# Performance work log

Hardware: AMD Instinct MI355X
Metric: run time of the kernel (lower is better)

Reference implementation:

```python
import jax, jax.numpy as jnp
import numpy as np
import math

B, N = 2, 384
TF, POS, TIME = 22, 32, 32
TPROJ = TIME + 1  # embed_fixed appends frame_mask channel
CS, CZ = 256, 128
POS_MAX, TIME_MAX = 2056.0, 10000.0
LN_EPS = 1e-5


def _index_emb(idx):
    # sinusoidal positional embedding of integer indices -> [..., POS]
    K = jnp.arange(POS // 2, dtype=jnp.float32)
    ang = idx[..., None].astype(jnp.float32) * jnp.pi / (POS_MAX ** (2.0 * K / POS))
    return jnp.concatenate([jnp.sin(ang), jnp.cos(ang)], axis=-1)


def _time_emb(t):
    # standard score-sde timestep embedding -> [M, TIME]
    half = TIME // 2
    freqs = jnp.exp(-(math.log(TIME_MAX) / (half - 1)) * jnp.arange(half, dtype=jnp.float32))
    ang = t[:, None] * freqs[None, :]
    return jnp.concatenate([jnp.sin(ang), jnp.cos(ang)], axis=-1)


def _ln(x, g, b):
    m = jnp.mean(x, axis=-1, keepdims=True)
    v = jnp.var(x, axis=-1, keepdims=True)
    return (x - m) * jax.lax.rsqrt(v + LN_EPS) * g + b


def _lin(x, W, b):
    return x @ W.T + b


def _forward(seq_idx, seq_feat, timestep, frame_mask,
             W_npos, b_npos, W_ntf, b_ntf, W_ntime, b_ntime,
             W_n1, b_n1, W_n2, b_n2, g_n, be_n,
             W_epos, b_epos, W_etf, b_etf, W_etime, b_etime,
             W_e1, b_e1, W_e2, b_e2, g_e, be_e):
    Bn, Nn = seq_idx.shape
    rel = seq_idx[:, :, None] - seq_idx[:, None, :]  # [B,N,N]
    seq_emb = _lin(_index_emb(seq_idx), W_npos, b_npos)          # [B,N,CS]
    edge_emb = _lin(_index_emb(rel), W_epos, b_epos)             # [B,N,N,CZ]
    seq_emb = seq_emb + _lin(seq_feat, W_ntf, b_ntf)
    # _cross_concat(x) @ W^T == (x @ Wl^T)[:, :, None] + (x @ Wr^T)[:, None, :] + b
    # (same math, avoids the O(N^2 * 2*TF) concatenated intermediate)
    edge_emb = edge_emb + (seq_feat @ W_etf[:, :TF].T)[:, :, None, :] \
                        + (seq_feat @ W_etf[:, TF:].T)[:, None, :, :] + b_etf
    t_res = (timestep[:, None] * frame_mask).reshape(-1)
    temb = _time_emb(t_res).reshape(Bn, Nn, TIME)
    temb = jnp.concatenate([temb, frame_mask[..., None]], axis=-1)  # embed_fixed -> TPROJ
    seq_emb = seq_emb + _lin(temb, W_ntime, b_ntime)
    edge_emb = edge_emb + (temb @ W_etime[:, :TPROJ].T)[:, :, None, :] \
                        + (temb @ W_etime[:, TPROJ:].T)[:, None, :, :] + b_etime
    # node_embedder: ReLU -> Linear -> ReLU -> Linear -> LayerNorm
    h = _lin(jax.nn.relu(seq_emb), W_n1, b_n1)
    seq_emb = _ln(_lin(jax.nn.relu(h), W_n2, b_n2), g_n, be_n)
    h = _lin(jax.nn.relu(edge_emb), W_e1, b_e1)
    edge_emb = _ln(_lin(jax.nn.relu(h), W_e2, b_e2), g_e, be_e)
    return seq_emb, edge_emb


def setup_inputs() -> dict:
    key = jax.random.key(0)
    ks = jax.random.split(key, 20)
    inp = {
        'seq_idx': jnp.sort(jax.random.randint(ks[0], (B, N), 0, 1000), axis=-1),
        'seq_feat': jax.random.normal(ks[1], (B, N, TF), dtype=jnp.float32),
        'timestep': jax.random.uniform(ks[2], (B,), dtype=jnp.float32),
        'frame_mask': jnp.ones((B, N), dtype=jnp.float32),
    }
    def lin(k, o, i):
        return 0.02 * jax.random.normal(k, (o, i), dtype=jnp.float32), jnp.zeros((o,), jnp.float32)
    inp['W_npos'], inp['b_npos'] = lin(ks[3], CS, POS)
    inp['W_ntf'], inp['b_ntf'] = lin(ks[4], CS, TF)
    inp['W_ntime'], inp['b_ntime'] = lin(ks[5], CS, TPROJ)
    inp['W_n1'], inp['b_n1'] = lin(ks[6], CS, CS)
    inp['W_n2'], inp['b_n2'] = lin(ks[7], CS, CS)
    inp['g_n'], inp['be_n'] = jnp.ones((CS,), jnp.float32), jnp.zeros((CS,), jnp.float32)
    inp['W_epos'], inp['b_epos'] = lin(ks[8], CZ, POS)
    inp['W_etf'], inp['b_etf'] = lin(ks[9], CZ, 2 * TF)
    inp['W_etime'], inp['b_etime'] = lin(ks[10], CZ, 2 * TPROJ)
    inp['W_e1'], inp['b_e1'] = lin(ks[11], CZ, CZ)
    inp['W_e2'], inp['b_e2'] = lin(ks[12], CZ, CZ)
    inp['g_e'], inp['be_e'] = jnp.ones((CZ,), jnp.float32), jnp.zeros((CZ,), jnp.float32)
    return inp


def reference(seq_idx, seq_feat, timestep, frame_mask,
              W_npos, b_npos, W_ntf, b_ntf, W_ntime, b_ntime,
              W_n1, b_n1, W_n2, b_n2, g_n, be_n,
              W_epos, b_epos, W_etf, b_etf, W_etime, b_etime,
              W_e1, b_e1, W_e2, b_e2, g_e, be_e):
    return _forward(seq_idx, seq_feat, timestep, frame_mask,
                    W_npos, b_npos, W_ntf, b_ntf, W_ntime, b_ntime,
                    W_n1, b_n1, W_n2, b_n2, g_n, be_n,
                    W_epos, b_epos, W_etf, b_etf, W_etime, b_etime,
                    W_e1, b_e1, W_e2, b_e2, g_e, be_e)
```

## Files before the change

kernel.cpp:

```cpp
#include <hip/hip_runtime.h>
#include <hip/hip_bf16.h>

#define BB 2
#define NN 384
#define TFD 22
#define POSD 32
#define TPROJ 33
#define CS 256
#define CZ 128
#define PI_F 3.14159265358979323846f

typedef __hip_bfloat16 bf16;
typedef __attribute__((ext_vector_type(8))) short short8;
typedef __attribute__((ext_vector_type(4))) float floatx4;

__device__ __forceinline__ float bfbits2f(unsigned short u) {
  unsigned v = ((unsigned)u) << 16;
  float f;
  __builtin_memcpy(&f, &v, 4);
  return f;
}
__device__ __forceinline__ unsigned short f2bf(float x) {
  bf16 h = __float2bfloat16(x);
  unsigned short u;
  __builtin_memcpy(&u, &h, 2);
  return u;
}
__device__ __forceinline__ bool probe_f32(const void* fm) {
  return *(const unsigned*)fm == 0x3F800000u;
}

#define TAB_OFF 0
#define SEQ0_OFF 262144
#define EL_OFF 458752
#define ER_OFF 557056
#define P_OFF 655360
#define WB_OFF 716288
#define pSEQF 0
#define pTS 16896
#define pFM 16898
#define pWNPOS 17666
#define pBNPOS 25858
#define pWNTF 26114
#define pBNTF 31746
#define pWNTIME 32002
#define pBNTIME 40450
#define pBN1 40706
#define pBN2 40962
#define pGN 41218
#define pBEN 41474
#define pWEPOS 41730
#define pBEPOS 45826
#define pWETF 45954
#define pBETF 51586
#define pWETIME 51714
#define pBETIME 60162
#define pBE1 60290
#define pBE2 60418
#define pGE 60546
#define pBEE 60674
#define UB_WE1 0
#define UB_WE2 16384
#define UB_WN1 32768
#define UB_WN2 98304

struct InPtrs { const void* p[28]; };

__global__ void cvt_all(InPtrs ip, float* __restrict__ ws) {
  const int idx = blockIdx.x * 256 + threadIdx.x;
  if (idx >= 224642) return;
  const int srci[27] = {1,2,3,4,5,6,7,8,9,11,13,14,15,16,17,18,19,20,21,23,25,26,27,22,24,10,12};
  const int pre[28] = {0,16896,16898,17666,25858,26114,31746,32002,40450,40706,40962,41218,41474,
                       41730,45826,45954,51586,51714,60162,60290,60418,60546,60674,60802,
                       77186,93570,159106,224642};
  const bool f32 = probe_f32(ip.p[3]);
  int e = 0;
  while (idx >= pre[e + 1]) ++e;
  const int j = idx - pre[e];
  const void* sp = ip.p[srci[e]];
  if (e < 23) {
    float v = f32 ? ((const float*)sp)[j] : bfbits2f(((const unsigned short*)sp)[j]);
    ws[P_OFF + pre[e] + j] = v;
  } else {
    const int ub[4] = {UB_WE1, UB_WE2, UB_WN1, UB_WN2};
    unsigned short* wb = (unsigned short*)(ws + WB_OFF);
    wb[ub[e - 23] + j] = f32 ? f2bf(((const float*)sp)[j]) : ((const unsigned short*)sp)[j];
  }
}

__global__ void tab_kernel(float* __restrict__ ws) {
  const float* P = ws + P_OFF;
  __shared__ float pe[POSD];
  int r = blockIdx.x, t = threadIdx.x;
  if (t < 16) {
    float ang = (float)(r - 1024) * PI_F * powf(2056.0f, -(float)t * (1.0f / 16.0f));
    pe[t] = sinf(ang);
    pe[t + 16] = cosf(ang);
  }
  __syncthreads();
  float acc = P[pBEPOS + t] + P[pBETF + t] + P[pBETIME + t];
  const float* w = P + pWEPOS + t * POSD;
#pragma unroll
  for (int k = 0; k < POSD; ++k) acc += pe[k] * w[k];
  ws[TAB_OFF + r * CZ + t] = acc;
}

__global__ void nodeprep(const int* __restrict__ seq_idx, float* __restrict__ ws) {
  const float* P = ws + P_OFF;
  __shared__ float pe[POSD];
  __shared__ float temb[TPROJ];
  __shared__ float sf[TFD];
  int bn = blockIdx.x, t = threadIdx.x;
  int b = bn / NN;
  float fm = P[pFM + bn];
  if (t < 16) {
    float idxv = (float)seq_idx[bn];
    float ang = idxv * PI_F * powf(2056.0f, -(float)t * (1.0f / 16.0f));
    pe[t] = sinf(ang);
    pe[t + 16] = cosf(ang);
    float tres = P[pTS + b] * fm;
    float freq = expf(-(logf(10000.0f) * (1.0f / 15.0f)) * (float)t);
    temb[t] = sinf(tres * freq);
    temb[t + 16] = cosf(tres * freq);
  }
  if (t == 16) temb[32] = fm;
  if (t < TFD) sf[t] = P[pSEQF + bn * TFD + t];
  __syncthreads();
  {
    int c = t;
    float acc = P[pBNPOS + c] + P[pBNTF + c] + P[pBNTIME + c];
    const float* w = P + pWNPOS + c * POSD;
#pragma unroll
    for (int k = 0; k < POSD; ++k) acc += pe[k] * w[k];
    const float* w2 = P + pWNTF + c * TFD;
#pragma unroll
    for (int k = 0; k < TFD; ++k) acc += sf[k] * w2[k];
    const float* w3 = P + pWNTIME + c * TPROJ;
#pragma unroll
    for (int k = 0; k < TPROJ; ++k) acc += temb[k] * w3[k];
    ws[SEQ0_OFF + bn * CS + c] = acc;
  }
  if (t < CZ) {
    int c = t;
    float acc = 0.0f;
    const float* w = P + pWETF + c * (2 * TFD);
#pragma unroll
    for (int k = 0; k < TFD; ++k) acc += sf[k] * w[k];
    const float* w2 = P + pWETIME + c * (2 * TPROJ);
#pragma unroll
    for (int k = 0; k < TPROJ; ++k) acc += temb[k] * w2[k];
    ws[EL_OFF + bn * CZ + c] = acc;
  } else {
    int c = t - CZ;
    float acc = 0.0f;
    const float* w = P + pWETF + c * (2 * TFD) + TFD;
#pragma unroll
    for (int k = 0; k < TFD; ++k) acc += sf[k] * w[k];
    const float* w2 = P + pWETIME + c * (2 * TPROJ) + TPROJ;
#pragma unroll
    for (int k = 0; k < TPROJ; ++k) acc += temb[k] * w2[k];
    ws[ER_OFF + bn * CZ + c] = acc;
  }
}

__global__ __launch_bounds__(256) void node_mfma(const float* __restrict__ ws,
                                                 const void* __restrict__ fmraw,
                                                 void* __restrict__ outv) {
  __shared__ __align__(16) unsigned short sA0[32][CS + 8];
  __shared__ __align__(16) unsigned short sA1[32][CS + 8];
  __shared__ float sO[32][CS + 4];
  __shared__ float sRed[32][8], sRedQ[32][8], sMu[32], sRs[32];
  const float* P = ws + P_OFF;
  const unsigned short* WB = (const unsigned short*)(ws + WB_OFF);
  const unsigned short* W1 = WB + UB_WN1;
  const unsigned short* W2 = WB + UB_WN2;
  const int row0 = blockIdx.x * 32;
  const int t = threadIdx.x;
  const int wave = t >> 6, lane = t & 63, quad = lane >> 4, l16 = lane & 15;
  {
    const float* seq0 = ws + SEQ0_OFF;
#pragma unroll
    for (int r = 0; r < 32; ++r) sA0[r][t] = f2bf(fmaxf(seq0[(row0 + r) * CS + t], 0.0f));
  }
  __syncthreads();
  short8 af[2][8];
  floatx4 acc[2][4];
#pragma unroll
  for (int mt = 0; mt < 2; ++mt)
#pragma unroll
    for (int ks = 0; ks < 8; ++ks)
      af[mt][ks] = *(const short8*)&sA0[mt * 16 + l16][ks * 32 + quad * 8];
#pragma unroll
  for (int mt = 0; mt < 2; ++mt)
#pragma unroll
    for (int n = 0; n < 4; ++n) acc[mt][n] = (floatx4){0.f, 0.f, 0.f, 0.f};
#pragma unroll
  for (int ntl = 0; ntl < 4; ++ntl) {
    int n0 = (wave * 4 + ntl) * 16;
#pragma unroll
    for (int ks = 0; ks < 8; ++ks) {
      short8 bfr = *(const short8*)&W1[(n0 + l16) * CS + ks * 32 + quad * 8];
      acc[0][ntl] = __builtin_amdgcn_mfma_f32_16x16x32_bf16(af[0][ks], bfr, acc[0][ntl], 0, 0, 0);
      acc[1][ntl] = __builtin_amdgcn_mfma_f32_16x16x32_bf16(af[1][ks], bfr, acc[1][ntl], 0, 0, 0);
    }
  }
#pragma unroll
  for (int ntl = 0; ntl < 4; ++ntl) {
    int n0 = (wave * 4 + ntl) * 16;
    float b1v = P[pBN1 + n0 + l16];
#pragma unroll
    for (int mt = 0; mt < 2; ++mt)
#pragma unroll
      for (int i = 0; i < 4; ++i)
        sA1[mt * 16 + quad * 4 + i][n0 + l16] = f2bf(fmaxf(acc[mt][ntl][i] + b1v, 0.0f));
  }
  __syncthreads();
#pragma unroll
  for (int mt = 0; mt < 2; ++mt)
#pragma unroll
    for (int ks = 0; ks < 8; ++ks)
      af[mt][ks] = *(const short8*)&sA1[mt * 16 + l16][ks * 32 + quad * 8];
#pragma unroll
  for (int mt = 0; mt < 2; ++mt)
#pragma unroll
    for (int n = 0; n < 4; ++n) acc[mt][n] = (floatx4){0.f, 0.f, 0.f, 0.f};
#pragma unroll
  for (int ntl = 0; ntl < 4; ++ntl) {
    int n0 = (wave * 4 + ntl) * 16;
#pragma unroll
    for (int ks = 0; ks < 8; ++ks) {
      short8 bfr = *(const short8*)&W2[(n0 + l16) * CS + ks * 32 + quad * 8];
      acc[0][ntl] = __builtin_amdgcn_mfma_f32_16x16x32_bf16(af[0][ks], bfr, acc[0][ntl], 0, 0, 0);
      acc[1][ntl] = __builtin_amdgcn_mfma_f32_16x16x32_bf16(af[1][ks], bfr, acc[1][ntl], 0, 0, 0);
    }
  }
#pragma unroll
  for (int ntl = 0; ntl < 4; ++ntl) {
    int n0 = (wave * 4 + ntl) * 16;
    float b2v = P[pBN2 + n0 + l16];
#pragma unroll
    for (int mt = 0; mt < 2; ++mt)
#pragma unroll
      for (int i = 0; i < 4; ++i)
        sO[mt * 16 + quad * 4 + i][n0 + l16] = acc[mt][ntl][i] + b2v;
  }
  __syncthreads();
  {
    int r = t >> 3, seg = t & 7;
    float s = 0.f, q = 0.f;
#pragma unroll
    for (int k = 0; k < 32; ++k) { float v = sO[r][seg * 32 + k]; s += v; q += v * v; }
    sRed[r][seg] = s; sRedQ[r][seg] = q;
  }
  __syncthreads();
  if (t < 32) {
    float s = 0.f, q = 0.f;
#pragma unroll
    for (int k = 0; k < 8; ++k) { s += sRed[t][k]; q += sRedQ[t][k]; }
    float mu = s * (1.0f / CS);
    float var = q * (1.0f / CS) - mu * mu;
    sMu[t] = mu; sRs[t] = rsqrtf(var + 1e-5f);
  }
  __syncthreads();
  {
    float g = P[pGN + t], be = P[pBEN + t];
    if (probe_f32(fmraw)) {
      float* o = (float*)outv;
#pragma unroll
      for (int r = 0; r < 32; ++r)
        o[(size_t)(row0 + r) * CS + t] = (sO[r][t] - sMu[r]) * sRs[r] * g + be;
    } else {
      bf16* o = (bf16*)outv;
#pragma unroll
      for (int r = 0; r < 32; ++r)
        o[(size_t)(row0 + r) * CS + t] = __float2bfloat16((sO[r][t] - sMu[r]) * sRs[r] * g + be);
    }
  }
}

__global__ __launch_bounds__(256) void edge_mfma(const int* __restrict__ seq_idx,
                                                 const float* __restrict__ ws,
                                                 const void* __restrict__ fmraw,
                                                 void* __restrict__ outv) {
  __shared__ __align__(16) unsigned short sA0[32][CZ + 8];
  __shared__ __align__(16) unsigned short sA1[32][CZ + 8];
  __shared__ float sO[32][CZ + 4];
  __shared__ int sRel[32];
  __shared__ float sRed[32][8], sRedQ[32][8], sMu[32], sRs[32];
  const float* tab = ws + TAB_OFF;
  const float* eL = ws + EL_OFF;
  const float* eR = ws + ER_OFF;
  const float* P = ws + P_OFF;
  const unsigned short* WB = (const unsigned short*)(ws + WB_OFF);
  const unsigned short* W1 = WB + UB_WE1;
  const unsigned short* W2 = WB + UB_WE2;
  const int bid = blockIdx.x;
  const int jt = bid % (NN / 32);
  const int rem = bid / (NN / 32);
  const int irow = rem % NN;
  const int b = rem / NN;
  const int j0 = jt * 32;
  const int t = threadIdx.x;
  const int wave = t >> 6, lane = t & 63, quad = lane >> 4, l16 = lane & 15;
  if (t < 32) {
    int rel = seq_idx[b * NN + irow] - seq_idx[b * NN + j0 + t] + 1024;
    sRel[t] = min(max(rel, 0), 2047);
  }
  __syncthreads();
  {
    int c = t & 127, rh = (t >> 7) * 16;
    float eLi = eL[(b * NN + irow) * CZ + c];
#pragma unroll
    for (int rr = 0; rr < 16; ++rr) {
      int r = rh + rr;
      float v = tab[sRel[r] * CZ + c] + eLi + eR[(b * NN + j0 + r) * CZ + c];
      sA0[r][c] = f2bf(fmaxf(v, 0.0f));
    }
  }
  __syncthreads();
  short8 af[2][4];
  floatx4 acc[2][2];
#pragma unroll
  for (int mt = 0; mt < 2; ++mt)
#pragma unroll
    for (int ks = 0; ks < 4; ++ks)
      af[mt][ks] = *(const short8*)&sA0[mt * 16 + l16][ks * 32 + quad * 8];
#pragma unroll
  for (int mt = 0; mt < 2; ++mt)
#pragma unroll
    for (int n = 0; n < 2; ++n) acc[mt][n] = (floatx4){0.f, 0.f, 0.f, 0.f};
#pragma unroll
  for (int ntl = 0; ntl < 2; ++ntl) {
    int n0 = (wave * 2 + ntl) * 16;
#pragma unroll
    for (int ks = 0; ks < 4; ++ks) {
      short8 bfr = *(const short8*)&W1[(n0 + l16) * CZ + ks * 32 + quad * 8];
      acc[0][ntl] = __builtin_amdgcn_mfma_f32_16x16x32_bf16(af[0][ks], bfr, acc[0][ntl], 0, 0, 0);
      acc[1][ntl] = __builtin_amdgcn_mfma_f32_16x16x32_bf16(af[1][ks], bfr, acc[1][ntl], 0, 0, 0);
    }
  }
#pragma unroll
  for (int ntl = 0; ntl < 2; ++ntl) {
    int n0 = (wave * 2 + ntl) * 16;
    float b1v = P[pBE1 + n0 + l16];
#pragma unroll
    for (int mt = 0; mt < 2; ++mt)
#pragma unroll
      for (int i = 0; i < 4; ++i)
        sA1[mt * 16 + quad * 4 + i][n0 + l16] = f2bf(fmaxf(acc[mt][ntl][i] + b1v, 0.0f));
  }
  __syncthreads();
#pragma unroll
  for (int mt = 0; mt < 2; ++mt)
#pragma unroll
    for (int ks = 0; ks < 4; ++ks)
      af[mt][ks] = *(const short8*)&sA1[mt * 16 + l16][ks * 32 + quad * 8];
#pragma unroll
  for (int mt = 0; mt < 2; ++mt)
#pragma unroll
    for (int n = 0; n < 2; ++n) acc[mt][n] = (floatx4){0.f, 0.f, 0.f, 0.f};
#pragma unroll
  for (int ntl = 0; ntl < 2; ++ntl) {
    int n0 = (wave * 2 + ntl) * 16;
#pragma unroll
    for (int ks = 0; ks < 4; ++ks) {
      short8 bfr = *(const short8*)&W2[(n0 + l16) * CZ + ks * 32 + quad * 8];
      acc[0][ntl] = __builtin_amdgcn_mfma_f32_16x16x32_bf16(af[0][ks], bfr, acc[0][ntl], 0, 0, 0);
      acc[1][ntl] = __builtin_amdgcn_mfma_f32_16x16x32_bf16(af[1][ks], bfr, acc[1][ntl], 0, 0, 0);
    }
  }
#pragma unroll
  for (int ntl = 0; ntl < 2; ++ntl) {
    int n0 = (wave * 2 + ntl) * 16;
    float b2v = P[pBE2 + n0 + l16];
#pragma unroll
    for (int mt = 0; mt < 2; ++mt)
#pragma unroll
      for (int i = 0; i < 4; ++i)
        sO[mt * 16 + quad * 4 + i][n0 + l16] = acc[mt][ntl][i] + b2v;
  }
  __syncthreads();
  {
    int r = t >> 3, seg = t & 7;
    float s = 0.f, q = 0.f;
#pragma unroll
    for (int k = 0; k < 16; ++k) { float v = sO[r][seg * 16 + k]; s += v; q += v * v; }
    sRed[r][seg] = s; sRedQ[r][seg] = q;
  }
  __syncthreads();
  if (t < 32) {
    float s = 0.f, q = 0.f;
#pragma unroll
    for (int k = 0; k < 8; ++k) { s += sRed[t][k]; q += sRedQ[t][k]; }
    float mu = s * (1.0f / CZ);
    float var = q * (1.0f / CZ) - mu * mu;
    sMu[t] = mu; sRs[t] = rsqrtf(var + 1e-5f);
  }
  __syncthreads();
  {
    int c = t & 127, rh = (t >> 7) * 16;
    float g = P[pGE + c], be = P[pBEE + c];
    size_t base = ((size_t)(b * NN + irow) * NN + j0) * CZ + c;
    if (probe_f32(fmraw)) {
      float* o = (float*)outv + (size_t)BB * NN * CS;
#pragma unroll
      for (int rr = 0; rr < 16; ++rr) {
        int r = rh + rr;
        o[base + (size_t)r * CZ] = (sO[r][c] - sMu[r]) * sRs[r] * g + be;
      }
    } else {
      bf16* o = (bf16*)outv + (size_t)BB * NN * CS;
#pragma unroll
      for (int rr = 0; rr < 16; ++rr) {
        int r = rh + rr;
        o[base + (size_t)r * CZ] = __float2bfloat16((sO[r][c] - sMu[r]) * sRs[r] * g + be);
      }
    }
  }
}

extern "C" void kernel_launch(void* const* d_in, const int* in_sizes, int n_in,
                              void* d_out, int out_size, void* d_ws, size_t ws_size,
                              hipStream_t stream) {
  (void)in_sizes; (void)n_in; (void)out_size; (void)ws_size;
  const int* seq_idx = (const int*)d_in[0];
  float* ws = (float*)d_ws;
  InPtrs ip;
  for (int i = 0; i < 28; ++i) ip.p[i] = d_in[i];
  hipLaunchKernelGGL(cvt_all, dim3(878), dim3(256), 0, stream, ip, ws);
  hipLaunchKernelGGL(tab_kernel, dim3(2048), dim3(CZ), 0, stream, ws);
  hipLaunchKernelGGL(nodeprep, dim3(BB * NN), dim3(CS), 0, stream, seq_idx, ws);
  hipLaunchKernelGGL(node_mfma, dim3(BB * NN / 32), dim3(256), 0, stream, ws, d_in[3], d_out);
  hipLaunchKernelGGL(edge_mfma, dim3(BB * NN * (NN / 32)), dim3(256), 0, stream,
                     seq_idx, ws, d_in[3], d_out);
}
```

Before: 308.4 us.

## Merge prep kernels into one launch and restructure edge MLP per-wave in registers

Folds the conversion, relative-position table and node-prep kernels into a single launch. Tab and nodeprep now read raw inputs directly instead of waiting on the converted workspace copy. The edge kernel is restructured so each wave owns 16 pair rows: it builds the MFMA operands straight from global float4 loads, keeps the hidden layer in a small per-wave LDS tile, and does the LayerNorm with wave shuffles and vectorised stores. This removes block-wide syncs and shared staging, at the cost of more registers per thread and re-reading the weights from global memory in every wave.

```diff
diff --git a/kernel.cpp b/kernel.cpp
--- a/kernel.cpp
+++ b/kernel.cpp
@@ -28,6 +28,9 @@
 }
 __device__ __forceinline__ bool probe_f32(const void* fm) {
   return *(const unsigned*)fm == 0x3F800000u;
+}
+__device__ __forceinline__ float ldraw(const void* p, int i, bool f32) {
+  return f32 ? ((const float*)p)[i] : bfbits2f(((const unsigned short*)p)[i]);
 }
 
 #define TAB_OFF 0
@@ -64,102 +67,103 @@
 #define UB_WN1 32768
 #define UB_WN2 98304
 
+#define NB_CVT 878
+#define NB_TAB 1024
+#define NB_NODEPREP 768
+
 struct InPtrs { const void* p[28]; };
 
-__global__ void cvt_all(InPtrs ip, float* __restrict__ ws) {
-  const int idx = blockIdx.x * 256 + threadIdx.x;
-  if (idx >= 224642) return;
-  const int srci[27] = {1,2,3,4,5,6,7,8,9,11,13,14,15,16,17,18,19,20,21,23,25,26,27,22,24,10,12};
-  const int pre[28] = {0,16896,16898,17666,25858,26114,31746,32002,40450,40706,40962,41218,41474,
-                       41730,45826,45954,51586,51714,60162,60290,60418,60546,60674,60802,
-                       77186,93570,159106,224642};
+__device__ const int g_srci[27] = {1,2,3,4,5,6,7,8,9,11,13,14,15,16,17,18,19,20,21,23,25,26,27,22,24,10,12};
+__device__ const int g_pre[28] = {0,16896,16898,17666,25858,26114,31746,32002,40450,40706,40962,41218,41474,
+                                  41730,45826,45954,51586,51714,60162,60290,60418,60546,60674,60802,
+                                  77186,93570,159106,224642};
+__device__ const int g_ub[4] = {UB_WE1, UB_WE2, UB_WN1, UB_WN2};
+
+__global__ __launch_bounds__(256) void prep(InPtrs ip, const int* __restrict__ seq_idx,
+                                            float* __restrict__ ws) {
   const bool f32 = probe_f32(ip.p[3]);
-  int e = 0;
-  while (idx >= pre[e + 1]) ++e;
-  const int j = idx - pre[e];
-  const void* sp = ip.p[srci[e]];
-  if (e < 23) {
-    float v = f32 ? ((const float*)sp)[j] : bfbits2f(((const unsigned short*)sp)[j]);
-    ws[P_OFF + pre[e] + j] = v;
-  } else {
-    const int ub[4] = {UB_WE1, UB_WE2, UB_WN1, UB_WN2};
-    unsigned short* wb = (unsigned short*)(ws + WB_OFF);
-    wb[ub[e - 23] + j] = f32 ? f2bf(((const float*)sp)[j]) : ((const unsigned short*)sp)[j];
-  }
-}
-
-__global__ void tab_kernel(float* __restrict__ ws) {
-  const float* P = ws + P_OFF;
-  __shared__ float pe[POSD];
-  int r = blockIdx.x, t = threadIdx.x;
-  if (t < 16) {
-    float ang = (float)(r - 1024) * PI_F * powf(2056.0f, -(float)t * (1.0f / 16.0f));
-    pe[t] = sinf(ang);
-    pe[t + 16] = cosf(ang);
-  }
-  __syncthreads();
-  float acc = P[pBEPOS + t] + P[pBETF + t] + P[pBETIME + t];
-  const float* w = P + pWEPOS + t * POSD;
-#pragma unroll
-  for (int k = 0; k < POSD; ++k) acc += pe[k] * w[k];
-  ws[TAB_OFF + r * CZ + t] = acc;
-}
-
-__global__ void nodeprep(const int* __restrict__ seq_idx, float* __restrict__ ws) {
-  const float* P = ws + P_OFF;
-  __shared__ float pe[POSD];
-  __shared__ float temb[TPROJ];
-  __shared__ float sf[TFD];
-  int bn = blockIdx.x, t = threadIdx.x;
-  int b = bn / NN;
-  float fm = P[pFM + bn];
-  if (t < 16) {
-    float idxv = (float)seq_idx[bn];
-    float ang = idxv * PI_F * powf(2056.0f, -(float)t * (1.0f / 16.0f));
-    pe[t] = sinf(ang);
-    pe[t + 16] = cosf(ang);
-    float tres = P[pTS + b] * fm;
-    float freq = expf(-(logf(10000.0f) * (1.0f / 15.0f)) * (float)t);
-    temb[t] = sinf(tres * freq);
-    temb[t + 16] = cosf(tres * freq);
-  }
-  if (t == 16) temb[32] = fm;
-  if (t < TFD) sf[t] = P[pSEQF + bn * TFD + t];
-  __syncthreads();
+  const int t = threadIdx.x;
+  int sb = blockIdx.x;
+  if (sb < NB_CVT) {
+    int idx = sb * 256 + t;
+    if (idx >= 224642) return;
+    int e = 0;
+    while (idx >= g_pre[e + 1]) ++e;
+    int j = idx - g_pre[e];
+    const void* sp = ip.p[g_srci[e]];
+    if (e < 23) {
+      ws[P_OFF + g_pre[e] + j] = ldraw(sp, j, f32);
+    } else {
+      unsigned short* wb = (unsigned short*)(ws + WB_OFF);
+      wb[g_ub[e - 23] + j] = f32 ? f2bf(((const float*)sp)[j]) : ((const unsigned short*)sp)[j];
+    }
+    return;
+  }
+  sb -= NB_CVT;
+  if (sb < NB_TAB) {
+    __shared__ float pe[2][POSD];
+    int half = t >> 7, tc = t & 127;
+    int r = sb * 2 + half;
+    if (tc < 16) {
+      float ang = (float)(r - 1024) * PI_F * powf(2056.0f, -(float)tc * (1.0f / 16.0f));
+      pe[half][tc] = sinf(ang);
+      pe[half][tc + 16] = cosf(ang);
+    }
+    __syncthreads();
+    float acc = ldraw(ip.p[17], tc, f32) + ldraw(ip.p[19], tc, f32) + ldraw(ip.p[21], tc, f32);
+#pragma unroll
+    for (int k = 0; k < POSD; ++k) acc += pe[half][k] * ldraw(ip.p[16], tc * POSD + k, f32);
+    ws[TAB_OFF + r * CZ + tc] = acc;
+    return;
+  }
+  sb -= NB_TAB;
   {
-    int c = t;
-    float acc = P[pBNPOS + c] + P[pBNTF + c] + P[pBNTIME + c];
-    const float* w = P + pWNPOS + c * POSD;
-#pragma unroll
-    for (int k = 0; k < POSD; ++k) acc += pe[k] * w[k];
-    const float* w2 = P + pWNTF + c * TFD;
-#pragma unroll
-    for (int k = 0; k < TFD; ++k) acc += sf[k] * w2[k];
-    const float* w3 = P + pWNTIME + c * TPROJ;
-#pragma unroll
-    for (int k = 0; k < TPROJ; ++k) acc += temb[k] * w3[k];
-    ws[SEQ0_OFF + bn * CS + c] = acc;
-  }
-  if (t < CZ) {
-    int c = t;
-    float acc = 0.0f;
-    const float* w = P + pWETF + c * (2 * TFD);
-#pragma unroll
-    for (int k = 0; k < TFD; ++k) acc += sf[k] * w[k];
-    const float* w2 = P + pWETIME + c * (2 * TPROJ);
-#pragma unroll
-    for (int k = 0; k < TPROJ; ++k) acc += temb[k] * w2[k];
-    ws[EL_OFF + bn * CZ + c] = acc;
-  } else {
-    int c = t - CZ;
-    float acc = 0.0f;
-    const float* w = P + pWETF + c * (2 * TFD) + TFD;
-#pragma unroll
-    for (int k = 0; k < TFD; ++k) acc += sf[k] * w[k];
-    const float* w2 = P + pWETIME + c * (2 * TPROJ) + TPROJ;
-#pragma unroll
-    for (int k = 0; k < TPROJ; ++k) acc += temb[k] * w2[k];
-    ws[ER_OFF + bn * CZ + c] = acc;
+    __shared__ float pe[POSD];
+    __shared__ float temb[TPROJ];
+    __shared__ float sf[TFD];
+    int bn = sb, b = bn / NN;
+    float fm = ldraw(ip.p[3], bn, f32);
+    if (t < 16) {
+      float idxv = (float)seq_idx[bn];
+      float ang = idxv * PI_F * powf(2056.0f, -(float)t * (1.0f / 16.0f));
+      pe[t] = sinf(ang);
+      pe[t + 16] = cosf(ang);
+      float tres = ldraw(ip.p[2], b, f32) * fm;
+      float freq = expf(-(logf(10000.0f) * (1.0f / 15.0f)) * (float)t);
+      temb[t] = sinf(tres * freq);
+      temb[t + 16] = cosf(tres * freq);
+    }
+    if (t == 16) temb[32] = fm;
+    if (t < TFD) sf[t] = ldraw(ip.p[1], bn * TFD + t, f32);
+    __syncthreads();
+    {
+      int c = t;
+      float acc = ldraw(ip.p[5], c, f32) + ldraw(ip.p[7], c, f32) + ldraw(ip.p[9], c, f32);
+#pragma unroll
+      for (int k = 0; k < POSD; ++k) acc += pe[k] * ldraw(ip.p[4], c * POSD + k, f32);
+#pragma unroll
+      for (int k = 0; k < TFD; ++k) acc += sf[k] * ldraw(ip.p[6], c * TFD + k, f32);
+#pragma unroll
+      for (int k = 0; k < TPROJ; ++k) acc += temb[k] * ldraw(ip.p[8], c * TPROJ + k, f32);
+      ws[SEQ0_OFF + bn * CS + c] = acc;
+    }
+    if (t < CZ) {
+      int c = t;
+      float acc = 0.0f;
+#pragma unroll
+      for (int k = 0; k < TFD; ++k) acc += sf[k] * ldraw(ip.p[18], c * (2 * TFD) + k, f32);
+#pragma unroll
+      for (int k = 0; k < TPROJ; ++k) acc += temb[k] * ldraw(ip.p[20], c * (2 * TPROJ) + k, f32);
+      ws[EL_OFF + bn * CZ + c] = acc;
+    } else {
+      int c = t - CZ;
+      float acc = 0.0f;
+#pragma unroll
+      for (int k = 0; k < TFD; ++k) acc += sf[k] * ldraw(ip.p[18], c * (2 * TFD) + TFD + k, f32);
+#pragma unroll
+      for (int k = 0; k < TPROJ; ++k) acc += temb[k] * ldraw(ip.p[20], c * (2 * TPROJ) + TPROJ + k, f32);
+      ws[ER_OFF + bn * CZ + c] = acc;
+    }
   }
 }
 
@@ -282,139 +286,123 @@
                                                  const float* __restrict__ ws,
                                                  const void* __restrict__ fmraw,
                                                  void* __restrict__ outv) {
-  __shared__ __align__(16) unsigned short sA0[32][CZ + 8];
-  __shared__ __align__(16) unsigned short sA1[32][CZ + 8];
-  __shared__ float sO[32][CZ + 4];
-  __shared__ int sRel[32];
-  __shared__ float sRed[32][8], sRedQ[32][8], sMu[32], sRs[32];
+  __shared__ unsigned short H2[4][16][136];
   const float* tab = ws + TAB_OFF;
   const float* eL = ws + EL_OFF;
   const float* eR = ws + ER_OFF;
   const float* P = ws + P_OFF;
-  const unsigned short* WB = (const unsigned short*)(ws + WB_OFF);
-  const unsigned short* W1 = WB + UB_WE1;
-  const unsigned short* W2 = WB + UB_WE2;
+  const unsigned short* W1 = (const unsigned short*)(ws + WB_OFF) + UB_WE1;
+  const unsigned short* W2 = (const unsigned short*)(ws + WB_OFF) + UB_WE2;
   const int bid = blockIdx.x;
-  const int jt = bid % (NN / 32);
-  const int rem = bid / (NN / 32);
+  const int jt = bid % (NN / 64);
+  const int rem = bid / (NN / 64);
   const int irow = rem % NN;
   const int b = rem / NN;
-  const int j0 = jt * 32;
   const int t = threadIdx.x;
-  const int wave = t >> 6, lane = t & 63, quad = lane >> 4, l16 = lane & 15;
-  if (t < 32) {
-    int rel = seq_idx[b * NN + irow] - seq_idx[b * NN + j0 + t] + 1024;
-    sRel[t] = min(max(rel, 0), 2047);
-  }
-  __syncthreads();
-  {
-    int c = t & 127, rh = (t >> 7) * 16;
-    float eLi = eL[(b * NN + irow) * CZ + c];
-#pragma unroll
-    for (int rr = 0; rr < 16; ++rr) {
-      int r = rh + rr;
-      float v = tab[sRel[r] * CZ + c] + eLi + eR[(b * NN + j0 + r) * CZ + c];
-      sA0[r][c] = f2bf(fmaxf(v, 0.0f));
-    }
-  }
-  __syncthreads();
-  short8 af[2][4];
-  floatx4 acc[2][2];
-#pragma unroll
-  for (int mt = 0; mt < 2; ++mt)
-#pragma unroll
-    for (int ks = 0; ks < 4; ++ks)
-      af[mt][ks] = *(const short8*)&sA0[mt * 16 + l16][ks * 32 + quad * 8];
-#pragma unroll
-  for (int mt = 0; mt < 2; ++mt)
-#pragma unroll
-    for (int n = 0; n < 2; ++n) acc[mt][n] = (floatx4){0.f, 0.f, 0.f, 0.f};
-#pragma unroll
-  for (int ntl = 0; ntl < 2; ++ntl) {
-    int n0 = (wave * 2 + ntl) * 16;
+  const int w = t >> 6, lane = t & 63, quad = lane >> 4, l16 = lane & 15;
+  const int j = jt * 64 + w * 16 + l16;
+  int rel = seq_idx[b * NN + irow] - seq_idx[b * NN + j] + 1024;
+  rel = min(max(rel, 0), 2047);
+  union U8 { short8 v; unsigned short u[8]; };
+  short8 af[4];
+  const float* tabr = tab + rel * CZ;
+  const float* eRr = eR + (b * NN + j) * CZ;
+  const float* eLr = eL + (b * NN + irow) * CZ;
+#pragma unroll
+  for (int ks = 0; ks < 4; ++ks) {
+    int c0 = ks * 32 + quad * 8;
+    float4 t0 = *(const float4*)(tabr + c0), t1 = *(const float4*)(tabr + c0 + 4);
+    float4 r0 = *(const float4*)(eRr + c0), r1 = *(const float4*)(eRr + c0 + 4);
+    float4 l0 = *(const float4*)(eLr + c0), l1 = *(const float4*)(eLr + c0 + 4);
+    U8 a;
+    a.u[0] = f2bf(fmaxf(t0.x + r0.x + l0.x, 0.f));
+    a.u[1] = f2bf(fmaxf(t0.y + r0.y + l0.y, 0.f));
+    a.u[2] = f2bf(fmaxf(t0.z + r0.z + l0.z, 0.f));
+    a.u[3] = f2bf(fmaxf(t0.w + r0.w + l0.w, 0.f));
+    a.u[4] = f2bf(fmaxf(t1.x + r1.x + l1.x, 0.f));
+    a.u[5] = f2bf(fmaxf(t1.y + r1.y + l1.y, 0.f));
+    a.u[6] = f2bf(fmaxf(t1.z + r1.z + l1.z, 0.f));
+    a.u[7] = f2bf(fmaxf(t1.w + r1.w + l1.w, 0.f));
+    af[ks] = a.v;
+  }
+  floatx4 acc1[8];
+#pragma unroll
+  for (int mt = 0; mt < 8; ++mt) {
+    acc1[mt] = (floatx4){0.f, 0.f, 0.f, 0.f};
 #pragma unroll
     for (int ks = 0; ks < 4; ++ks) {
-      short8 bfr = *(const short8*)&W1[(n0 + l16) * CZ + ks * 32 + quad * 8];
-      acc[0][ntl] = __builtin_amdgcn_mfma_f32_16x16x32_bf16(af[0][ks], bfr, acc[0][ntl], 0, 0, 0);
-      acc[1][ntl] = __builtin_amdgcn_mfma_f32_16x16x32_bf16(af[1][ks], bfr, acc[1][ntl], 0, 0, 0);
-    }
-  }
-#pragma unroll
-  for (int ntl = 0; ntl < 2; ++ntl) {
-    int n0 = (wave * 2 + ntl) * 16;
-    float b1v = P[pBE1 + n0 + l16];
-#pragma unroll
-    for (int mt = 0; mt < 2; ++mt)
-#pragma unroll
-      for (int i = 0; i < 4; ++i)
-        sA1[mt * 16 + quad * 4 + i][n0 + l16] = f2bf(fmaxf(acc[mt][ntl][i] + b1v, 0.0f));
-  }
-  __syncthreads();
-#pragma unroll
-  for (int mt = 0; mt < 2; ++mt)
-#pragma unroll
-    for (int ks = 0; ks < 4; ++ks)
-      af[mt][ks] = *(const short8*)&sA1[mt * 16 + l16][ks * 32 + quad * 8];
-#pragma unroll
-  for (int mt = 0; mt < 2; ++mt)
-#pragma unroll
-    for (int n = 0; n < 2; ++n) acc[mt][n] = (floatx4){0.f, 0.f, 0.f, 0.f};
-#pragma unroll
-  for (int ntl = 0; ntl < 2; ++ntl) {
-    int n0 = (wave * 2 + ntl) * 16;
+      short8 wf = *(const short8*)&W1[(mt * 16 + l16) * CZ + ks * 32 + quad * 8];
+      acc1[mt] = __builtin_amdgcn_mfma_f32_16x16x32_bf16(wf, af[ks], acc1[mt], 0, 0, 0);
+    }
+  }
+#pragma unroll
+  for (int mt = 0; mt < 8; ++mt) {
+    float4 b1 = *(const float4*)&P[pBE1 + mt * 16 + quad * 4];
+    unsigned u0 = f2bf(fmaxf(acc1[mt][0] + b1.x, 0.f));
+    unsigned u1 = f2bf(fmaxf(acc1[mt][1] + b1.y, 0.f));
+    unsigned u2 = f2bf(fmaxf(acc1[mt][2] + b1.z, 0.f));
+    unsigned u3 = f2bf(fmaxf(acc1[mt][3] + b1.w, 0.f));
+    uint2 pk;
+    pk.x = u0 | (u1 << 16);
+    pk.y = u2 | (u3 << 16);
+    *(uint2*)&H2[w][l16][mt * 16 + quad * 4] = pk;
+  }
+  short8 bf2[4];
+#pragma unroll
+  for (int ks = 0; ks < 4; ++ks)
+    bf2[ks] = *(const short8*)&H2[w][l16][ks * 32 + quad * 8];
+  floatx4 acc2[8];
+#pragma unroll
+  for (int mt = 0; mt < 8; ++mt) {
+    acc2[mt] = (floatx4){0.f, 0.f, 0.f, 0.f};
 #pragma unroll
     for (int ks = 0; ks < 4; ++ks) {
-      short8 bfr = *(const short8*)&W2[(n0 + l16) * CZ + ks * 32 + quad * 8];
-      acc[0][ntl] = __builtin_amdgcn_mfma_f32_16x16x32_bf16(af[0][ks], bfr, acc[0][ntl], 0, 0, 0);
-      acc[1][ntl] = __builtin_amdgcn_mfma_f32_16x16x32_bf16(af[1][ks], bfr, acc[1][ntl], 0, 0, 0);
-    }
-  }
-#pragma unroll
-  for (int ntl = 0; ntl < 2; ++ntl) {
-    int n0 = (wave * 2 + ntl) * 16;
-    float b2v = P[pBE2 + n0 + l16];
-#pragma unroll
-    for (int mt = 0; mt < 2; ++mt)
-#pragma unroll
-      for (int i = 0; i < 4; ++i)
-        sO[mt * 16 + quad * 4 + i][n0 + l16] = acc[mt][ntl][i] + b2v;
-  }
-  __syncthreads();
-  {
-    int r = t >> 3, seg = t & 7;
-    float s = 0.f, q = 0.f;
-#pragma unroll
-    for (int k = 0; k < 16; ++k) { float v = sO[r][seg * 16 + k]; s += v; q += v * v; }
-    sRed[r][seg] = s; sRedQ[r][seg] = q;
-  }
-  __syncthreads();
-  if (t < 32) {
-    float s = 0.f, q = 0.f;
-#pragma unroll
-    for (int k = 0; k < 8; ++k) { s += sRed[t][k]; q += sRedQ[t][k]; }
-    float mu = s * (1.0f / CZ);
-    float var = q * (1.0f / CZ) - mu * mu;
-    sMu[t] = mu; sRs[t] = rsqrtf(var + 1e-5f);
-  }
-  __syncthreads();
-  {
-    int c = t & 127, rh = (t >> 7) * 16;
-    float g = P[pGE + c], be = P[pBEE + c];
-    size_t base = ((size_t)(b * NN + irow) * NN + j0) * CZ + c;
-    if (probe_f32(fmraw)) {
-      float* o = (float*)outv + (size_t)BB * NN * CS;
-#pragma unroll
-      for (int rr = 0; rr < 16; ++rr) {
-        int r = rh + rr;
-        o[base + (size_t)r * CZ] = (sO[r][c] - sMu[r]) * sRs[r] * g + be;
-      }
-    } else {
-      bf16* o = (bf16*)outv + (size_t)BB * NN * CS;
-#pragma unroll
-      for (int rr = 0; rr < 16; ++rr) {
-        int r = rh + rr;
-        o[base + (size_t)r * CZ] = __float2bfloat16((sO[r][c] - sMu[r]) * sRs[r] * g + be);
-      }
+      short8 wf = *(const short8*)&W2[(mt * 16 + l16) * CZ + ks * 32 + quad * 8];
+      acc2[mt] = __builtin_amdgcn_mfma_f32_16x16x32_bf16(wf, bf2[ks], acc2[mt], 0, 0, 0);
+    }
+  }
+  float s = 0.f, q = 0.f;
+#pragma unroll
+  for (int mt = 0; mt < 8; ++mt) {
+    float4 b2 = *(const float4*)&P[pBE2 + mt * 16 + quad * 4];
+    acc2[mt][0] += b2.x; acc2[mt][1] += b2.y; acc2[mt][2] += b2.z; acc2[mt][3] += b2.w;
+#pragma unroll
+    for (int i = 0; i < 4; ++i) { float v = acc2[mt][i]; s += v; q += v * v; }
+  }
+  s += __shfl_xor(s, 16, 64); q += __shfl_xor(q, 16, 64);
+  s += __shfl_xor(s, 32, 64); q += __shfl_xor(q, 32, 64);
+  float mu = s * (1.0f / CZ);
+  float rs = rsqrtf(q * (1.0f / CZ) - mu * mu + 1e-5f);
+  size_t base = ((size_t)(b * NN + irow) * NN + j) * CZ;
+  if (probe_f32(fmraw)) {
+    float* o = (float*)outv + (size_t)BB * NN * CS;
+#pragma unroll
+    for (int mt = 0; mt < 8; ++mt) {
+      int c0 = mt * 16 + quad * 4;
+      float4 g4 = *(const float4*)&P[pGE + c0];
+      float4 be4 = *(const float4*)&P[pBEE + c0];
+      float4 o4;
+      o4.x = (acc2[mt][0] - mu) * rs * g4.x + be4.x;
+      o4.y = (acc2[mt][1] - mu) * rs * g4.y + be4.y;
+      o4.z = (acc2[mt][2] - mu) * rs * g4.z + be4.z;
+      o4.w = (acc2[mt][3] - mu) * rs * g4.w + be4.w;
+      *(float4*)(o + base + c0) = o4;
+    }
+  } else {
+    unsigned short* o = (unsigned short*)outv + (size_t)BB * NN * CS;
+#pragma unroll
+    for (int mt = 0; mt < 8; ++mt) {
+      int c0 = mt * 16 + quad * 4;
+      float4 g4 = *(const float4*)&P[pGE + c0];
+      float4 be4 = *(const float4*)&P[pBEE + c0];
+      unsigned u0 = f2bf((acc2[mt][0] - mu) * rs * g4.x + be4.x);
+      unsigned u1 = f2bf((acc2[mt][1] - mu) * rs * g4.y + be4.y);
+      unsigned u2 = f2bf((acc2[mt][2] - mu) * rs * g4.z + be4.z);
+      unsigned u3 = f2bf((acc2[mt][3] - mu) * rs * g4.w + be4.w);
+      uint2 pk;
+      pk.x = u0 | (u1 << 16);
+      pk.y = u2 | (u3 << 16);
+      *(uint2*)(o + base + c0) = pk;
     }
   }
 }
@@ -427,10 +415,9 @@
   float* ws = (float*)d_ws;
   InPtrs ip;
   for (int i = 0; i < 28; ++i) ip.p[i] = d_in[i];
-  hipLaunchKernelGGL(cvt_all, dim3(878), dim3(256), 0, stream, ip, ws);
-  hipLaunchKernelGGL(tab_kernel, dim3(2048), dim3(CZ), 0, stream, ws);
-  hipLaunchKernelGGL(nodeprep, dim3(BB * NN), dim3(CS), 0, stream, seq_idx, ws);
+  hipLaunchKernelGGL(prep, dim3(NB_CVT + NB_TAB + NB_NODEPREP), dim3(256), 0, stream,
+                     ip, seq_idx, ws);
+  hipLaunchKernelGGL(edge_mfma, dim3(BB * NN * (NN / 64)), dim3(256), 0, stream,
+                     seq_idx, ws, d_in[3], d_out);
   hipLaunchKernelGGL(node_mfma, dim3(BB * NN / 32), dim3(256), 0, stream, ws, d_in[3], d_out);
-  hipLaunchKernelGGL(edge_mfma, dim3(BB * NN * (NN / 32)), dim3(256), 0, stream,
-                     seq_idx, ws, d_in[3], d_out);
-}
+}
```

Result: slower. 438.1 us (+42.1%).
